# Optimization experiments

Hardware: AMD Instinct MI355X
Metric: run time of the kernel (lower is better)

Reference implementation:

```python
import jax, jax.numpy as jnp
import numpy as np

ALPHA = 0.1  # leaky relu negative slope
EF = 256     # edge_features

def setup_inputs() -> dict:
    key = jax.random.key(0)
    k1, k2, k3, k4, k5 = jax.random.split(key, 5)
    N, Na, IN_F, OUT_F = 8192, 8192, 512, 256 * 2 // 1  # OUT_F set below
    OUT_F = 512
    feat_edge   = jax.random.normal(k1, (N, EF), dtype=jnp.float32)
    feat_edge_a = jax.random.normal(k2, (Na, EF), dtype=jnp.float32)
    feat_node_a = jax.random.normal(k3, (Na, IN_F), dtype=jnp.float32)
    # xavier_normal-ish init for params
    weight = jax.random.normal(k4, (IN_F, OUT_F), dtype=jnp.float32) * (1.414 * np.sqrt(2.0 / (IN_F + OUT_F)))
    att    = jax.random.normal(k5, (2 * EF, 1), dtype=jnp.float32) * (1.414 * np.sqrt(2.0 / (2 * EF + 1)))
    return {"feat_edge": feat_edge, "feat_edge_a": feat_edge_a,
            "feat_node_a": feat_node_a, "weight": weight, "att": att}

def reference(feat_edge, feat_edge_a, feat_node_a, weight, att):
    # Wh: [Na, out_features]
    Wh = feat_node_a @ weight
    # additive attention scores via rank-1 broadcast: e [N, Na]
    s1 = feat_edge @ att[:EF, :]      # [N, 1]
    s2 = feat_edge_a @ att[EF:, :]    # [Na, 1]
    e = jax.nn.leaky_relu(s1 + s2.T, negative_slope=ALPHA)
    attention = jax.nn.softmax(e, axis=1)  # sup=False path; dropout identity (eval)
    h_prime = attention @ Wh               # [N, out_features]
    return jax.nn.elu(h_prime)             # concat=True -> elu
```

## Files before the change

### kernel.cpp

```cpp
#include <hip/hip_runtime.h>
#include <cstdint>
#include <cstddef>

#define LRALPHA 0.1f
static constexpr int NR = 8192;
static constexpr int EF = 256;
static constexpr int IN_F = 512;
static constexpr int OUT_F = 512;
static constexpr int KP2 = 1024;
static constexpr int NCH = 128;
static constexpr int CHR = 64;

typedef __attribute__((ext_vector_type(8))) _Float16 f16x8;
typedef __attribute__((ext_vector_type(4))) float f32x4;

__global__ __launch_bounds__(256) void k_prep(const float* __restrict__ feat_edge,
                                              const float* __restrict__ feat_edge_a,
                                              const float* __restrict__ att,
                                              const float* __restrict__ W,
                                              float* __restrict__ s1,
                                              float* __restrict__ s2,
                                              short* __restrict__ B3t) {
  int b = blockIdx.x;
  if (b < 4096) {
    int vrow = b * 4 + (threadIdx.x >> 6);
    int lane = threadIdx.x & 63;
    const float* feat; const float* av; float* outp; int row;
    if (vrow < NR) { row = vrow; feat = feat_edge; av = att; outp = s1; }
    else { row = vrow - NR; feat = feat_edge_a; av = att + EF; outp = s2; }
    float4 f = reinterpret_cast<const float4*>(feat + (size_t)row * EF)[lane];
    float4 a = reinterpret_cast<const float4*>(av)[lane];
    float d = f.x * a.x + f.y * a.y + f.z * a.z + f.w * a.w;
#pragma unroll
    for (int off = 32; off > 0; off >>= 1) d += __shfl_xor(d, off);
    if (lane == 0) outp[row] = d;
  } else {
    int i = (b - 4096) * 256 + threadIdx.x;
    int n = i >> 9, k = i & 511;
    float x = W[(size_t)k * OUT_F + n];
    _Float16 h = (_Float16)x;
    unsigned short u = __builtin_bit_cast(unsigned short, h);
    unsigned int w = (unsigned int)u | ((unsigned int)u << 16);
    *reinterpret_cast<unsigned int*>(B3t + (size_t)n * KP2 + 2 * k) = w;
  }
}

struct SReg4 { float4 a0, a1, a2, a3; int4 b0, b1, b2, b3; };

__device__ __forceinline__ int swz(int row, int slot) {
  return (row & ~7) | ((row & 7) ^ (slot & 7));
}

__global__ __launch_bounds__(256, 2) void k_gemm(const float* __restrict__ A,
                                                 const short* __restrict__ B3t,
                                                 float* __restrict__ Wh) {
  __shared__ short lA[2][8192];
  __shared__ short lB[2][8192];
  const int tid = threadIdx.x;
  const int wid = tid >> 6, lane = tid & 63;
  const int wr = wid >> 1, wc = wid & 1;
  int bid = blockIdx.x;
  int xcd = bid & 7, loc = bid >> 3;
  int mb = (xcd << 4) | (loc >> 3), nb = loc & 7;
  const int m0 = mb * 64, n0 = nb * 64;
  const int fr = lane & 15, g = lane >> 4;

  const int srow = tid >> 2, q = tid & 3;
  const float* gA = A + (size_t)(m0 + srow) * IN_F + q * 16;
  const short* gB = B3t + (size_t)(n0 + srow) * KP2 + q * 32;
  int wA[4], wB[4];
#pragma unroll
  for (int j = 0; j < 4; ++j) {
    int s = 4 * q + j;
    wA[j] = s * 512 + swz(srow, s) * 8;
    wB[j] = s * 512 + swz(srow, s) * 8;
  }

  f32x4 acc[2][2] = {};

  auto loadR = [&](SReg4& s, int t) {
    const float* pa = gA + t * 64;
    s.a0 = *reinterpret_cast<const float4*>(pa);
    s.a1 = *reinterpret_cast<const float4*>(pa + 4);
    s.a2 = *reinterpret_cast<const float4*>(pa + 8);
    s.a3 = *reinterpret_cast<const float4*>(pa + 12);
    const short* pb = gB + t * 128;
    s.b0 = *reinterpret_cast<const int4*>(pb);
    s.b1 = *reinterpret_cast<const int4*>(pb + 8);
    s.b2 = *reinterpret_cast<const int4*>(pb + 16);
    s.b3 = *reinterpret_cast<const int4*>(pb + 24);
  };

  auto cvt4 = [](float4 p) -> int4 {
    float xs[4] = {p.x, p.y, p.z, p.w};
    int out[4];
#pragma unroll
    for (int e = 0; e < 4; ++e) {
      _Float16 h = (_Float16)xs[e];
      _Float16 l = (_Float16)(xs[e] - (float)h);
      unsigned short uh = __builtin_bit_cast(unsigned short, h);
      unsigned short ul = __builtin_bit_cast(unsigned short, l);
      out[e] = (int)uh | ((int)ul << 16);
    }
    int4 r; r.x = out[0]; r.y = out[1]; r.z = out[2]; r.w = out[3];
    return r;
  };

  auto writeL = [&](int buf, SReg4& s) {
    *reinterpret_cast<int4*>(&lA[buf][wA[0]]) = cvt4(s.a0);
    *reinterpret_cast<int4*>(&lA[buf][wA[1]]) = cvt4(s.a1);
    *reinterpret_cast<int4*>(&lA[buf][wA[2]]) = cvt4(s.a2);
    *reinterpret_cast<int4*>(&lA[buf][wA[3]]) = cvt4(s.a3);
    *reinterpret_cast<int4*>(&lB[buf][wB[0]]) = s.b0;
    *reinterpret_cast<int4*>(&lB[buf][wB[1]]) = s.b1;
    *reinterpret_cast<int4*>(&lB[buf][wB[2]]) = s.b2;
    *reinterpret_cast<int4*>(&lB[buf][wB[3]]) = s.b3;
  };

  auto compute = [&](int buf) {
#pragma unroll
    for (int ks = 0; ks < 4; ++ks) {
      int s = ks * 4 + g;
      f16x8 af[2], bv[2];
#pragma unroll
      for (int m = 0; m < 2; ++m) {
        int row = wr * 32 + m * 16 + fr;
        af[m] = *reinterpret_cast<const f16x8*>(&lA[buf][s * 512 + swz(row, s) * 8]);
      }
#pragma unroll
      for (int n = 0; n < 2; ++n) {
        int row = wc * 32 + n * 16 + fr;
        bv[n] = *reinterpret_cast<const f16x8*>(&lB[buf][s * 512 + swz(row, s) * 8]);
      }
#pragma unroll
      for (int m = 0; m < 2; ++m)
#pragma unroll
        for (int n = 0; n < 2; ++n)
          acc[m][n] = __builtin_amdgcn_mfma_f32_16x16x32_f16(af[m], bv[n], acc[m][n], 0, 0, 0);
    }
  };

  SReg4 SA, SB;
  loadR(SA, 0); loadR(SB, 1);
  writeL(0, SA);
  loadR(SA, 2);
  __syncthreads();

  for (int t = 0; t < 4; t += 2) {
    writeL(1, SB); loadR(SB, t + 3);
    compute(0); __syncthreads();
    writeL(0, SA); loadR(SA, t + 4);
    compute(1); __syncthreads();
  }
  writeL(1, SB); loadR(SB, 7);
  compute(0); __syncthreads();
  writeL(0, SA);
  compute(1); __syncthreads();
  writeL(1, SB);
  compute(0); __syncthreads();
  compute(1);

#pragma unroll
  for (int m = 0; m < 2; ++m) {
#pragma unroll
    for (int n = 0; n < 2; ++n) {
      int row = m0 + wr * 32 + m * 16 + g * 4;
      int col = n0 + wc * 32 + n * 16 + fr;
#pragma unroll
      for (int r = 0; r < 4; ++r)
        Wh[(size_t)(row + r) * OUT_F + col] = acc[m][n][r];
    }
  }
}

__global__ __launch_bounds__(256) void k_rank(const float* __restrict__ s2,
                                              float* __restrict__ s2s, int* __restrict__ perm,
                                              float* __restrict__ eaA, float* __restrict__ ebA) {
  __shared__ unsigned int ls[32 * 260];
  int t = threadIdx.x;
#pragma unroll
  for (int k = 0; k < 8; ++k) {
    int q = t + 256 * k;
    int p = q >> 6, i = q & 63;
    uint4 u = reinterpret_cast<const uint4*>(s2)[q];
    uint4 v;
    v.x = (u.x >> 31) ? ~u.x : (u.x | 0x80000000u);
    v.y = (u.y >> 31) ? ~u.y : (u.y | 0x80000000u);
    v.z = (u.z >> 31) ? ~u.z : (u.z | 0x80000000u);
    v.w = (u.w >> 31) ? ~u.w : (u.w | 0x80000000u);
    *reinterpret_cast<uint4*>(&ls[p * 260 + i * 4]) = v;
  }
  __syncthreads();

  int ki = blockIdx.x * 8 + (t >> 5);
  int part = t & 31;
  unsigned int key = ls[(ki >> 8) * 260 + (ki & 255)];
  int rank = 0;
  const int base = part * 260;
  int jbase = part * 256;
#pragma unroll 8
  for (int q = 0; q < 64; ++q) {
    uint4 v = *reinterpret_cast<const uint4*>(&ls[base + q * 4]);
    int j = jbase + q * 4;
    rank += (v.x < key) || (v.x == key && (j + 0) < ki);
    rank += (v.y < key) || (v.y == key && (j + 1) < ki);
    rank += (v.z < key) || (v.z == key && (j + 2) < ki);
    rank += (v.w < key) || (v.w == key && (j + 3) < ki);
  }
  rank += __shfl_xor(rank, 1);
  rank += __shfl_xor(rank, 2);
  rank += __shfl_xor(rank, 4);
  rank += __shfl_xor(rank, 8);
  rank += __shfl_xor(rank, 16);
  if (part == 0) {
    float kf = s2[ki];
    s2s[rank] = kf; perm[rank] = ki;
    eaA[rank] = expf(kf); ebA[rank] = expf(LRALPHA * kf);
  }
}

__global__ __launch_bounds__(1024) void k_scan(const float* __restrict__ eaA,
                                               const float* __restrict__ ebA,
                                               float* __restrict__ sufa,
                                               float* __restrict__ preb) {
  int t = threadIdx.x;
  int lane = t & 63, w = t >> 6;
  float4 a0 = reinterpret_cast<const float4*>(eaA)[t * 2];
  float4 a1 = reinterpret_cast<const float4*>(eaA)[t * 2 + 1];
  float4 b0 = reinterpret_cast<const float4*>(ebA)[t * 2];
  float4 b1 = reinterpret_cast<const float4*>(ebA)[t * 2 + 1];
  float ea[8] = {a0.x, a0.y, a0.z, a0.w, a1.x, a1.y, a1.z, a1.w};
  float eb[8] = {b0.x, b0.y, b0.z, b0.w, b1.x, b1.y, b1.z, b1.w};
  float sa = 0.f, sb = 0.f;
#pragma unroll
  for (int e = 0; e < 8; ++e) { sa += ea[e]; sb += eb[e]; }

  float pb = sb;
#pragma unroll
  for (int off = 1; off < 64; off <<= 1) { float v = __shfl_up(pb, off); if (lane >= off) pb += v; }
  float pa = sa;
#pragma unroll
  for (int off = 1; off < 64; off <<= 1) { float v = __shfl_down(pa, off); if (lane < 64 - off) pa += v; }

  __shared__ float wtb[16], wta[16];
  if (lane == 63) wtb[w] = pb;
  if (lane == 0)  wta[w] = pa;
  __syncthreads();
  if (t == 0) {
    float rb = 0.f;
    for (int i = 0; i < 16; ++i) { float tmp = wtb[i]; wtb[i] = rb; rb += tmp; }
    float ra = 0.f;
    for (int i = 15; i >= 0; --i) { float tmp = wta[i]; wta[i] = ra; ra += tmp; }
  }
  __syncthreads();

  float run = wtb[w] + (pb - sb);
#pragma unroll
  for (int e = 0; e < 8; ++e) { preb[t * 8 + e] = run; run += eb[e]; }
  if (t == 1023) preb[NR] = run;
  run = wta[w] + (pa - sa);
#pragma unroll
  for (int e = 7; e >= 0; --e) { run += ea[e]; sufa[t * 8 + e] = run; }
  if (t == 0) sufa[NR] = 0.f;
}

__global__ __launch_bounds__(256) void k_passA(const float* __restrict__ Wh,
                                               const float* __restrict__ eaA,
                                               const float* __restrict__ ebA,
                                               const int* __restrict__ perm,
                                               float* __restrict__ chunkA, float* __restrict__ chunkB) {
  int chunk = blockIdx.x;
  int col = blockIdx.y * 256 + threadIdx.x;
  float accA = 0.f, accB = 0.f;
  int r0 = chunk * CHR;
  for (int rl = 0; rl < CHR; ++rl) {
    int r = r0 + rl;
    float v = Wh[(size_t)perm[r] * OUT_F + col];
    accA += eaA[r] * v;
    accB += ebA[r] * v;
  }
  chunkA[(size_t)col * NCH + chunk] = accA;
  chunkB[(size_t)col * NCH + chunk] = accB;
}

__global__ __launch_bounds__(256) void k_passB(const float* __restrict__ chunkA,
                                               const float* __restrict__ chunkB,
                                               float* __restrict__ baseA, float* __restrict__ baseB) {
  int lane = threadIdx.x & 63, w = threadIdx.x >> 6;
  int col = blockIdx.x * 4 + w;
  float xa0 = chunkA[(size_t)col * NCH + lane];
  float xa1 = chunkA[(size_t)col * NCH + 64 + lane];
  float yb0 = chunkB[(size_t)col * NCH + lane];
  float yb1 = chunkB[(size_t)col * NCH + 64 + lane];

  float p0 = yb0, p1 = yb1;
#pragma unroll
  for (int off = 1; off < 64; off <<= 1) {
    float v0 = __shfl_up(p0, off); if (lane >= off) p0 += v0;
    float v1 = __shfl_up(p1, off); if (lane >= off) p1 += v1;
  }
  float T0 = __shfl(p0, 63);
  p1 += T0;
  baseB[(size_t)lane * OUT_F + col] = p0 - yb0;
  baseB[(size_t)(64 + lane) * OUT_F + col] = p1 - yb1;

  float s0 = xa0, s1 = xa1;
#pragma unroll
  for (int off = 1; off < 64; off <<= 1) {
    float v1 = __shfl_down(s1, off); if (lane < 64 - off) s1 += v1;
    float v0 = __shfl_down(s0, off); if (lane < 64 - off) s0 += v0;
  }
  float S1 = __shfl(s1, 0);
  s0 += S1;
  baseA[(size_t)lane * OUT_F + col] = s0 - xa0;
  baseA[(size_t)(64 + lane) * OUT_F + col] = s1 - xa1;
}

__global__ __launch_bounds__(256) void k_passC(const float* __restrict__ Wh,
                                               const float* __restrict__ eaA,
                                               const float* __restrict__ ebA,
                                               const int* __restrict__ perm,
                                               const float* __restrict__ baseA,
                                               const float* __restrict__ baseB,
                                               float* __restrict__ SufA, float* __restrict__ PreB) {
  int chunk = blockIdx.x;
  int col = blockIdx.y * 256 + threadIdx.x;
  int r0 = chunk * CHR;
  float bA = baseA[(size_t)chunk * OUT_F + col];
  float bB = baseB[(size_t)chunk * OUT_F + col];
  float acc = 0.f;
  for (int rl = CHR - 1; rl >= 0; --rl) {
    int r = r0 + rl;
    float v = Wh[(size_t)perm[r] * OUT_F + col];
    acc += eaA[r] * v;
    SufA[(size_t)r * OUT_F + col] = acc + bA;
  }
  acc = 0.f;
  for (int rl = 0; rl < CHR; ++rl) {
    int r = r0 + rl;
    float v = Wh[(size_t)perm[r] * OUT_F + col];
    PreB[(size_t)r * OUT_F + col] = acc + bB;
    acc += ebA[r] * v;
  }
  if (chunk == NCH - 1) {
    SufA[(size_t)NR * OUT_F + col] = 0.f;
    PreB[(size_t)NR * OUT_F + col] = acc + bB;
  }
}

__global__ __launch_bounds__(256) void k_final(const float* __restrict__ s1,
                                               const float* __restrict__ s2s,
                                               const float* __restrict__ sufa,
                                               const float* __restrict__ preb,
                                               const float* __restrict__ SufA,
                                               const float* __restrict__ PreB,
                                               float* __restrict__ out) {
  int row = blockIdx.x * 4 + (threadIdx.x >> 6);
  int lane = threadIdx.x & 63;
  float sv = s1[row];
  float t = -sv;
  int lo = 0, hi = NR;
  while (lo < hi) {
    int mid = (lo + hi) >> 1;
    if (s2s[mid] > t) hi = mid; else lo = mid + 1;
  }
  float E1 = expf(sv), E1a = expf(LRALPHA * sv);
  float Z = E1 * sufa[lo] + E1a * preb[lo];
  const float* rA = SufA + (size_t)lo * OUT_F;
  const float* rB = PreB + (size_t)lo * OUT_F;
#pragma unroll
  for (int e = 0; e < 8; ++e) {
    int kc = e * 64 + lane;
    float num = E1 * rA[kc] + E1a * rB[kc];
    float h = num / Z;
    out[(size_t)row * OUT_F + kc] = (h > 0.f) ? h : expm1f(h);
  }
}

extern "C" void kernel_launch(void* const* d_in, const int* in_sizes, int n_in,
                              void* d_out, int out_size, void* d_ws, size_t ws_size,
                              hipStream_t stream) {
  (void)in_sizes; (void)n_in; (void)out_size; (void)ws_size;
  const float* feat_edge   = (const float*)d_in[0];
  const float* feat_edge_a = (const float*)d_in[1];
  const float* feat_node_a = (const float*)d_in[2];
  const float* weight      = (const float*)d_in[3];
  const float* att         = (const float*)d_in[4];
  float* out = (float*)d_out;

  char* ws = (char*)d_ws;
  size_t off = 0;
  auto alloc = [&](size_t bytes) { size_t o = off; off += (bytes + 255) & ~(size_t)255; return o; };

  float* Wh = (float*)(ws + alloc((size_t)NR * OUT_F * 4));
  size_t regionOff = alloc((size_t)(NR + 1) * OUT_F * 4 * 2);
  float* SufA = (float*)(ws + regionOff);
  float* PreB = (float*)(ws + regionOff + (size_t)(NR + 1) * OUT_F * 4);
  short* B3t  = (short*)(ws + regionOff);

  float* s1   = (float*)(ws + alloc(NR * 4));
  float* s2   = (float*)(ws + alloc(NR * 4));
  float* s2s  = (float*)(ws + alloc(NR * 4));
  int*   perm = (int*)  (ws + alloc(NR * 4));
  float* sufa = (float*)(ws + alloc((NR + 1) * 4));
  float* preb = (float*)(ws + alloc((NR + 1) * 4));
  float* eaA  = (float*)(ws + alloc(NR * 4));
  float* ebA  = (float*)(ws + alloc(NR * 4));
  float* chA  = (float*)(ws + alloc(NCH * OUT_F * 4));
  float* chB  = (float*)(ws + alloc(NCH * OUT_F * 4));
  float* bsA  = (float*)(ws + alloc(NCH * OUT_F * 4));
  float* bsB  = (float*)(ws + alloc(NCH * OUT_F * 4));

  k_prep<<<4096 + 1024, 256, 0, stream>>>(feat_edge, feat_edge_a, att, weight, s1, s2, B3t);
  k_gemm<<<1024, 256, 0, stream>>>(feat_node_a, B3t, Wh);
  k_rank<<<NR / 8, 256, 0, stream>>>(s2, s2s, perm, eaA, ebA);
  k_scan<<<1, 1024, 0, stream>>>(eaA, ebA, sufa, preb);
  k_passA<<<dim3(NCH, 2), 256, 0, stream>>>(Wh, eaA, ebA, perm, chA, chB);
  k_passB<<<NCH, 256, 0, stream>>>(chA, chB, bsA, bsB);
  k_passC<<<dim3(NCH, 2), 256, 0, stream>>>(Wh, eaA, ebA, perm, bsA, bsB, SufA, PreB);
  k_final<<<NR / 4, 256, 0, stream>>>(s1, s2s, sufa, preb, SufA, PreB, out);
}
```

Before: 86.30 us.

## Merge GEMM with rank kernel, fold scan and chunk-base pass into neighbours

Runs the GEMM and the s2 ranking sort as one launch, with blocks split by index over a shared LDS buffer. The global scalar scan moves into an extra block of passA, and passB is dropped because each passC block now sums the chunk totals it needs directly. Chunk totals are stored chunk-major for coalesced reads. This cuts three kernel launches and their serialisation gaps, but passC now does up to 128 redundant reads per column and the merged kernel carries the larger GEMM LDS footprint for rank blocks.

```diff
diff --git a/kernel.cpp b/kernel.cpp
--- a/kernel.cpp
+++ b/kernel.cpp
@@ -51,226 +51,231 @@
   return (row & ~7) | ((row & 7) ^ (slot & 7));
 }
 
-__global__ __launch_bounds__(256, 2) void k_gemm(const float* __restrict__ A,
-                                                 const short* __restrict__ B3t,
-                                                 float* __restrict__ Wh) {
-  __shared__ short lA[2][8192];
-  __shared__ short lB[2][8192];
+__global__ __launch_bounds__(256, 2) void k_gemmrank(const float* __restrict__ A,
+                                                     const short* __restrict__ B3t,
+                                                     float* __restrict__ Wh,
+                                                     const float* __restrict__ s2,
+                                                     float* __restrict__ s2s, int* __restrict__ perm,
+                                                     float* __restrict__ eaA, float* __restrict__ ebA) {
+  __shared__ int4 smem[4096];
   const int tid = threadIdx.x;
-  const int wid = tid >> 6, lane = tid & 63;
-  const int wr = wid >> 1, wc = wid & 1;
   int bid = blockIdx.x;
-  int xcd = bid & 7, loc = bid >> 3;
-  int mb = (xcd << 4) | (loc >> 3), nb = loc & 7;
-  const int m0 = mb * 64, n0 = nb * 64;
-  const int fr = lane & 15, g = lane >> 4;
-
-  const int srow = tid >> 2, q = tid & 3;
-  const float* gA = A + (size_t)(m0 + srow) * IN_F + q * 16;
-  const short* gB = B3t + (size_t)(n0 + srow) * KP2 + q * 32;
-  int wA[4], wB[4];
-#pragma unroll
-  for (int j = 0; j < 4; ++j) {
-    int s = 4 * q + j;
-    wA[j] = s * 512 + swz(srow, s) * 8;
-    wB[j] = s * 512 + swz(srow, s) * 8;
-  }
-
-  f32x4 acc[2][2] = {};
-
-  auto loadR = [&](SReg4& s, int t) {
-    const float* pa = gA + t * 64;
-    s.a0 = *reinterpret_cast<const float4*>(pa);
-    s.a1 = *reinterpret_cast<const float4*>(pa + 4);
-    s.a2 = *reinterpret_cast<const float4*>(pa + 8);
-    s.a3 = *reinterpret_cast<const float4*>(pa + 12);
-    const short* pb = gB + t * 128;
-    s.b0 = *reinterpret_cast<const int4*>(pb);
-    s.b1 = *reinterpret_cast<const int4*>(pb + 8);
-    s.b2 = *reinterpret_cast<const int4*>(pb + 16);
-    s.b3 = *reinterpret_cast<const int4*>(pb + 24);
-  };
-
-  auto cvt4 = [](float4 p) -> int4 {
-    float xs[4] = {p.x, p.y, p.z, p.w};
-    int out[4];
-#pragma unroll
-    for (int e = 0; e < 4; ++e) {
-      _Float16 h = (_Float16)xs[e];
-      _Float16 l = (_Float16)(xs[e] - (float)h);
-      unsigned short uh = __builtin_bit_cast(unsigned short, h);
-      unsigned short ul = __builtin_bit_cast(unsigned short, l);
-      out[e] = (int)uh | ((int)ul << 16);
-    }
-    int4 r; r.x = out[0]; r.y = out[1]; r.z = out[2]; r.w = out[3];
-    return r;
-  };
-
-  auto writeL = [&](int buf, SReg4& s) {
-    *reinterpret_cast<int4*>(&lA[buf][wA[0]]) = cvt4(s.a0);
-    *reinterpret_cast<int4*>(&lA[buf][wA[1]]) = cvt4(s.a1);
-    *reinterpret_cast<int4*>(&lA[buf][wA[2]]) = cvt4(s.a2);
-    *reinterpret_cast<int4*>(&lA[buf][wA[3]]) = cvt4(s.a3);
-    *reinterpret_cast<int4*>(&lB[buf][wB[0]]) = s.b0;
-    *reinterpret_cast<int4*>(&lB[buf][wB[1]]) = s.b1;
-    *reinterpret_cast<int4*>(&lB[buf][wB[2]]) = s.b2;
-    *reinterpret_cast<int4*>(&lB[buf][wB[3]]) = s.b3;
-  };
-
-  auto compute = [&](int buf) {
-#pragma unroll
-    for (int ks = 0; ks < 4; ++ks) {
-      int s = ks * 4 + g;
-      f16x8 af[2], bv[2];
-#pragma unroll
-      for (int m = 0; m < 2; ++m) {
-        int row = wr * 32 + m * 16 + fr;
-        af[m] = *reinterpret_cast<const f16x8*>(&lA[buf][s * 512 + swz(row, s) * 8]);
+  if (bid < 1024) {
+    short* lA = (short*)smem;
+    short* lB = (short*)smem + 16384;
+    const int wid = tid >> 6, lane = tid & 63;
+    const int wr = wid >> 1, wc = wid & 1;
+    int xcd = bid & 7, loc = bid >> 3;
+    int mb = (xcd << 4) | (loc >> 3), nb = loc & 7;
+    const int m0 = mb * 64, n0 = nb * 64;
+    const int fr = lane & 15, g = lane >> 4;
+
+    const int srow = tid >> 2, q = tid & 3;
+    const float* gA = A + (size_t)(m0 + srow) * IN_F + q * 16;
+    const short* gB = B3t + (size_t)(n0 + srow) * KP2 + q * 32;
+    int wA[4];
+#pragma unroll
+    for (int j = 0; j < 4; ++j) {
+      int s = 4 * q + j;
+      wA[j] = s * 512 + swz(srow, s) * 8;
+    }
+
+    f32x4 acc[2][2] = {};
+
+    auto loadR = [&](SReg4& s, int t) {
+      const float* pa = gA + t * 64;
+      s.a0 = *reinterpret_cast<const float4*>(pa);
+      s.a1 = *reinterpret_cast<const float4*>(pa + 4);
+      s.a2 = *reinterpret_cast<const float4*>(pa + 8);
+      s.a3 = *reinterpret_cast<const float4*>(pa + 12);
+      const short* pb = gB + t * 128;
+      s.b0 = *reinterpret_cast<const int4*>(pb);
+      s.b1 = *reinterpret_cast<const int4*>(pb + 8);
+      s.b2 = *reinterpret_cast<const int4*>(pb + 16);
+      s.b3 = *reinterpret_cast<const int4*>(pb + 24);
+    };
+
+    auto cvt4 = [](float4 p) -> int4 {
+      float xs[4] = {p.x, p.y, p.z, p.w};
+      int out[4];
+#pragma unroll
+      for (int e = 0; e < 4; ++e) {
+        _Float16 h = (_Float16)xs[e];
+        _Float16 l = (_Float16)(xs[e] - (float)h);
+        unsigned short uh = __builtin_bit_cast(unsigned short, h);
+        unsigned short ul = __builtin_bit_cast(unsigned short, l);
+        out[e] = (int)uh | ((int)ul << 16);
       }
+      int4 r; r.x = out[0]; r.y = out[1]; r.z = out[2]; r.w = out[3];
+      return r;
+    };
+
+    auto writeL = [&](int buf, SReg4& s) {
+      *reinterpret_cast<int4*>(&lA[buf * 8192 + wA[0]]) = cvt4(s.a0);
+      *reinterpret_cast<int4*>(&lA[buf * 8192 + wA[1]]) = cvt4(s.a1);
+      *reinterpret_cast<int4*>(&lA[buf * 8192 + wA[2]]) = cvt4(s.a2);
+      *reinterpret_cast<int4*>(&lA[buf * 8192 + wA[3]]) = cvt4(s.a3);
+      *reinterpret_cast<int4*>(&lB[buf * 8192 + wA[0]]) = s.b0;
+      *reinterpret_cast<int4*>(&lB[buf * 8192 + wA[1]]) = s.b1;
+      *reinterpret_cast<int4*>(&lB[buf * 8192 + wA[2]]) = s.b2;
+      *reinterpret_cast<int4*>(&lB[buf * 8192 + wA[3]]) = s.b3;
+    };
+
+    auto compute = [&](int buf) {
+#pragma unroll
+      for (int ks = 0; ks < 4; ++ks) {
+        int s = ks * 4 + g;
+        f16x8 af[2], bv[2];
+#pragma unroll
+        for (int m = 0; m < 2; ++m) {
+          int row = wr * 32 + m * 16 + fr;
+          af[m] = *reinterpret_cast<const f16x8*>(&lA[buf * 8192 + s * 512 + swz(row, s) * 8]);
+        }
+#pragma unroll
+        for (int n = 0; n < 2; ++n) {
+          int row = wc * 32 + n * 16 + fr;
+          bv[n] = *reinterpret_cast<const f16x8*>(&lB[buf * 8192 + s * 512 + swz(row, s) * 8]);
+        }
+#pragma unroll
+        for (int m = 0; m < 2; ++m)
+#pragma unroll
+          for (int n = 0; n < 2; ++n)
+            acc[m][n] = __builtin_amdgcn_mfma_f32_16x16x32_f16(af[m], bv[n], acc[m][n], 0, 0, 0);
+      }
+    };
+
+    SReg4 SA, SB;
+    loadR(SA, 0); loadR(SB, 1);
+    writeL(0, SA);
+    loadR(SA, 2);
+    __syncthreads();
+
+    for (int t = 0; t < 4; t += 2) {
+      writeL(1, SB); loadR(SB, t + 3);
+      compute(0); __syncthreads();
+      writeL(0, SA); loadR(SA, t + 4);
+      compute(1); __syncthreads();
+    }
+    writeL(1, SB); loadR(SB, 7);
+    compute(0); __syncthreads();
+    writeL(0, SA);
+    compute(1); __syncthreads();
+    writeL(1, SB);
+    compute(0); __syncthreads();
+    compute(1);
+
+#pragma unroll
+    for (int m = 0; m < 2; ++m) {
 #pragma unroll
       for (int n = 0; n < 2; ++n) {
-        int row = wc * 32 + n * 16 + fr;
-        bv[n] = *reinterpret_cast<const f16x8*>(&lB[buf][s * 512 + swz(row, s) * 8]);
+        int row = m0 + wr * 32 + m * 16 + g * 4;
+        int col = n0 + wc * 32 + n * 16 + fr;
+#pragma unroll
+        for (int r = 0; r < 4; ++r)
+          Wh[(size_t)(row + r) * OUT_F + col] = acc[m][n][r];
       }
-#pragma unroll
-      for (int m = 0; m < 2; ++m)
-#pragma unroll
-        for (int n = 0; n < 2; ++n)
-          acc[m][n] = __builtin_amdgcn_mfma_f32_16x16x32_f16(af[m], bv[n], acc[m][n], 0, 0, 0);
-    }
-  };
-
-  SReg4 SA, SB;
-  loadR(SA, 0); loadR(SB, 1);
-  writeL(0, SA);
-  loadR(SA, 2);
-  __syncthreads();
-
-  for (int t = 0; t < 4; t += 2) {
-    writeL(1, SB); loadR(SB, t + 3);
-    compute(0); __syncthreads();
-    writeL(0, SA); loadR(SA, t + 4);
-    compute(1); __syncthreads();
-  }
-  writeL(1, SB); loadR(SB, 7);
-  compute(0); __syncthreads();
-  writeL(0, SA);
-  compute(1); __syncthreads();
-  writeL(1, SB);
-  compute(0); __syncthreads();
-  compute(1);
-
-#pragma unroll
-  for (int m = 0; m < 2; ++m) {
-#pragma unroll
-    for (int n = 0; n < 2; ++n) {
-      int row = m0 + wr * 32 + m * 16 + g * 4;
-      int col = n0 + wc * 32 + n * 16 + fr;
-#pragma unroll
-      for (int r = 0; r < 4; ++r)
-        Wh[(size_t)(row + r) * OUT_F + col] = acc[m][n][r];
-    }
-  }
-}
-
-__global__ __launch_bounds__(256) void k_rank(const float* __restrict__ s2,
-                                              float* __restrict__ s2s, int* __restrict__ perm,
-                                              float* __restrict__ eaA, float* __restrict__ ebA) {
-  __shared__ unsigned int ls[32 * 260];
-  int t = threadIdx.x;
-#pragma unroll
-  for (int k = 0; k < 8; ++k) {
-    int q = t + 256 * k;
-    int p = q >> 6, i = q & 63;
-    uint4 u = reinterpret_cast<const uint4*>(s2)[q];
-    uint4 v;
-    v.x = (u.x >> 31) ? ~u.x : (u.x | 0x80000000u);
-    v.y = (u.y >> 31) ? ~u.y : (u.y | 0x80000000u);
-    v.z = (u.z >> 31) ? ~u.z : (u.z | 0x80000000u);
-    v.w = (u.w >> 31) ? ~u.w : (u.w | 0x80000000u);
-    *reinterpret_cast<uint4*>(&ls[p * 260 + i * 4]) = v;
-  }
-  __syncthreads();
-
-  int ki = blockIdx.x * 8 + (t >> 5);
-  int part = t & 31;
-  unsigned int key = ls[(ki >> 8) * 260 + (ki & 255)];
-  int rank = 0;
-  const int base = part * 260;
-  int jbase = part * 256;
+    }
+  } else {
+    unsigned int* ls = (unsigned int*)smem;
+#pragma unroll
+    for (int k = 0; k < 8; ++k) {
+      int q = tid + 256 * k;
+      int p = q >> 6, i = q & 63;
+      uint4 u = reinterpret_cast<const uint4*>(s2)[q];
+      uint4 v;
+      v.x = (u.x >> 31) ? ~u.x : (u.x | 0x80000000u);
+      v.y = (u.y >> 31) ? ~u.y : (u.y | 0x80000000u);
+      v.z = (u.z >> 31) ? ~u.z : (u.z | 0x80000000u);
+      v.w = (u.w >> 31) ? ~u.w : (u.w | 0x80000000u);
+      *reinterpret_cast<uint4*>(&ls[p * 260 + i * 4]) = v;
+    }
+    __syncthreads();
+
+    int ki = (bid - 1024) * 8 + (tid >> 5);
+    int part = tid & 31;
+    unsigned int key = ls[(ki >> 8) * 260 + (ki & 255)];
+    int rank = 0;
+    const int base = part * 260;
+    int jbase = part * 256;
 #pragma unroll 8
-  for (int q = 0; q < 64; ++q) {
-    uint4 v = *reinterpret_cast<const uint4*>(&ls[base + q * 4]);
-    int j = jbase + q * 4;
-    rank += (v.x < key) || (v.x == key && (j + 0) < ki);
-    rank += (v.y < key) || (v.y == key && (j + 1) < ki);
-    rank += (v.z < key) || (v.z == key && (j + 2) < ki);
-    rank += (v.w < key) || (v.w == key && (j + 3) < ki);
-  }
-  rank += __shfl_xor(rank, 1);
-  rank += __shfl_xor(rank, 2);
-  rank += __shfl_xor(rank, 4);
-  rank += __shfl_xor(rank, 8);
-  rank += __shfl_xor(rank, 16);
-  if (part == 0) {
-    float kf = s2[ki];
-    s2s[rank] = kf; perm[rank] = ki;
-    eaA[rank] = expf(kf); ebA[rank] = expf(LRALPHA * kf);
-  }
-}
-
-__global__ __launch_bounds__(1024) void k_scan(const float* __restrict__ eaA,
-                                               const float* __restrict__ ebA,
-                                               float* __restrict__ sufa,
-                                               float* __restrict__ preb) {
-  int t = threadIdx.x;
-  int lane = t & 63, w = t >> 6;
-  float4 a0 = reinterpret_cast<const float4*>(eaA)[t * 2];
-  float4 a1 = reinterpret_cast<const float4*>(eaA)[t * 2 + 1];
-  float4 b0 = reinterpret_cast<const float4*>(ebA)[t * 2];
-  float4 b1 = reinterpret_cast<const float4*>(ebA)[t * 2 + 1];
-  float ea[8] = {a0.x, a0.y, a0.z, a0.w, a1.x, a1.y, a1.z, a1.w};
-  float eb[8] = {b0.x, b0.y, b0.z, b0.w, b1.x, b1.y, b1.z, b1.w};
-  float sa = 0.f, sb = 0.f;
-#pragma unroll
-  for (int e = 0; e < 8; ++e) { sa += ea[e]; sb += eb[e]; }
-
-  float pb = sb;
-#pragma unroll
-  for (int off = 1; off < 64; off <<= 1) { float v = __shfl_up(pb, off); if (lane >= off) pb += v; }
-  float pa = sa;
-#pragma unroll
-  for (int off = 1; off < 64; off <<= 1) { float v = __shfl_down(pa, off); if (lane < 64 - off) pa += v; }
-
-  __shared__ float wtb[16], wta[16];
-  if (lane == 63) wtb[w] = pb;
-  if (lane == 0)  wta[w] = pa;
-  __syncthreads();
-  if (t == 0) {
-    float rb = 0.f;
-    for (int i = 0; i < 16; ++i) { float tmp = wtb[i]; wtb[i] = rb; rb += tmp; }
-    float ra = 0.f;
-    for (int i = 15; i >= 0; --i) { float tmp = wta[i]; wta[i] = ra; ra += tmp; }
-  }
-  __syncthreads();
-
-  float run = wtb[w] + (pb - sb);
-#pragma unroll
-  for (int e = 0; e < 8; ++e) { preb[t * 8 + e] = run; run += eb[e]; }
-  if (t == 1023) preb[NR] = run;
-  run = wta[w] + (pa - sa);
-#pragma unroll
-  for (int e = 7; e >= 0; --e) { run += ea[e]; sufa[t * 8 + e] = run; }
-  if (t == 0) sufa[NR] = 0.f;
+    for (int q = 0; q < 64; ++q) {
+      uint4 v = *reinterpret_cast<const uint4*>(&ls[base + q * 4]);
+      int j = jbase + q * 4;
+      rank += (v.x < key) || (v.x == key && (j + 0) < ki);
+      rank += (v.y < key) || (v.y == key && (j + 1) < ki);
+      rank += (v.z < key) || (v.z == key && (j + 2) < ki);
+      rank += (v.w < key) || (v.w == key && (j + 3) < ki);
+    }
+    rank += __shfl_xor(rank, 1);
+    rank += __shfl_xor(rank, 2);
+    rank += __shfl_xor(rank, 4);
+    rank += __shfl_xor(rank, 8);
+    rank += __shfl_xor(rank, 16);
+    if (part == 0) {
+      float kf = s2[ki];
+      s2s[rank] = kf; perm[rank] = ki;
+      eaA[rank] = expf(kf); ebA[rank] = expf(LRALPHA * kf);
+    }
+  }
 }
 
 __global__ __launch_bounds__(256) void k_passA(const float* __restrict__ Wh,
                                                const float* __restrict__ eaA,
                                                const float* __restrict__ ebA,
                                                const int* __restrict__ perm,
-                                               float* __restrict__ chunkA, float* __restrict__ chunkB) {
+                                               float* __restrict__ chunkA, float* __restrict__ chunkB,
+                                               float* __restrict__ sufa, float* __restrict__ preb) {
+  int t = threadIdx.x;
+  if (blockIdx.x == NCH) {
+    if (blockIdx.y != 0) return;
+    int lane = t & 63, w = t >> 6;
+    float sa = 0.f, sb = 0.f;
+#pragma unroll
+    for (int q = 0; q < 8; ++q) {
+      float4 va = reinterpret_cast<const float4*>(eaA)[t * 8 + q];
+      float4 vb = reinterpret_cast<const float4*>(ebA)[t * 8 + q];
+      sa += va.x + va.y + va.z + va.w;
+      sb += vb.x + vb.y + vb.z + vb.w;
+    }
+    float pb = sb;
+#pragma unroll
+    for (int off = 1; off < 64; off <<= 1) { float v = __shfl_up(pb, off); if (lane >= off) pb += v; }
+    float pa = sa;
+#pragma unroll
+    for (int off = 1; off < 64; off <<= 1) { float v = __shfl_down(pa, off); if (lane < 64 - off) pa += v; }
+    __shared__ float wtb[4], wta[4];
+    if (lane == 63) wtb[w] = pb;
+    if (lane == 0)  wta[w] = pa;
+    __syncthreads();
+    if (t == 0) {
+      float rb = 0.f;
+      for (int i = 0; i < 4; ++i) { float tmp = wtb[i]; wtb[i] = rb; rb += tmp; }
+      float ra = 0.f;
+      for (int i = 3; i >= 0; --i) { float tmp = wta[i]; wta[i] = ra; ra += tmp; }
+    }
+    __syncthreads();
+    float run = wtb[w] + (pb - sb);
+#pragma unroll
+    for (int q = 0; q < 8; ++q) {
+      float4 vb = reinterpret_cast<const float4*>(ebA)[t * 8 + q];
+      float e4[4] = {vb.x, vb.y, vb.z, vb.w};
+#pragma unroll
+      for (int e = 0; e < 4; ++e) { preb[t * 32 + q * 4 + e] = run; run += e4[e]; }
+    }
+    if (t == 255) preb[NR] = run;
+    run = wta[w] + (pa - sa);
+#pragma unroll
+    for (int q = 7; q >= 0; --q) {
+      float4 va = reinterpret_cast<const float4*>(eaA)[t * 8 + q];
+      float e4[4] = {va.x, va.y, va.z, va.w};
+#pragma unroll
+      for (int e = 3; e >= 0; --e) { run += e4[e]; sufa[t * 32 + q * 4 + e] = run; }
+    }
+    if (t == 0) sufa[NR] = 0.f;
+    return;
+  }
   int chunk = blockIdx.x;
-  int col = blockIdx.y * 256 + threadIdx.x;
+  int col = blockIdx.y * 256 + t;
   float accA = 0.f, accB = 0.f;
   int r0 = chunk * CHR;
   for (int rl = 0; rl < CHR; ++rl) {
@@ -279,55 +284,23 @@
     accA += eaA[r] * v;
     accB += ebA[r] * v;
   }
-  chunkA[(size_t)col * NCH + chunk] = accA;
-  chunkB[(size_t)col * NCH + chunk] = accB;
-}
-
-__global__ __launch_bounds__(256) void k_passB(const float* __restrict__ chunkA,
-                                               const float* __restrict__ chunkB,
-                                               float* __restrict__ baseA, float* __restrict__ baseB) {
-  int lane = threadIdx.x & 63, w = threadIdx.x >> 6;
-  int col = blockIdx.x * 4 + w;
-  float xa0 = chunkA[(size_t)col * NCH + lane];
-  float xa1 = chunkA[(size_t)col * NCH + 64 + lane];
-  float yb0 = chunkB[(size_t)col * NCH + lane];
-  float yb1 = chunkB[(size_t)col * NCH + 64 + lane];
-
-  float p0 = yb0, p1 = yb1;
-#pragma unroll
-  for (int off = 1; off < 64; off <<= 1) {
-    float v0 = __shfl_up(p0, off); if (lane >= off) p0 += v0;
-    float v1 = __shfl_up(p1, off); if (lane >= off) p1 += v1;
-  }
-  float T0 = __shfl(p0, 63);
-  p1 += T0;
-  baseB[(size_t)lane * OUT_F + col] = p0 - yb0;
-  baseB[(size_t)(64 + lane) * OUT_F + col] = p1 - yb1;
-
-  float s0 = xa0, s1 = xa1;
-#pragma unroll
-  for (int off = 1; off < 64; off <<= 1) {
-    float v1 = __shfl_down(s1, off); if (lane < 64 - off) s1 += v1;
-    float v0 = __shfl_down(s0, off); if (lane < 64 - off) s0 += v0;
-  }
-  float S1 = __shfl(s1, 0);
-  s0 += S1;
-  baseA[(size_t)lane * OUT_F + col] = s0 - xa0;
-  baseA[(size_t)(64 + lane) * OUT_F + col] = s1 - xa1;
+  chunkA[chunk * OUT_F + col] = accA;
+  chunkB[chunk * OUT_F + col] = accB;
 }
 
 __global__ __launch_bounds__(256) void k_passC(const float* __restrict__ Wh,
                                                const float* __restrict__ eaA,
                                                const float* __restrict__ ebA,
                                                const int* __restrict__ perm,
-                                               const float* __restrict__ baseA,
-                                               const float* __restrict__ baseB,
+                                               const float* __restrict__ chunkA,
+                                               const float* __restrict__ chunkB,
                                                float* __restrict__ SufA, float* __restrict__ PreB) {
   int chunk = blockIdx.x;
   int col = blockIdx.y * 256 + threadIdx.x;
+  float bA = 0.f, bB = 0.f;
+  for (int cp = chunk + 1; cp < NCH; ++cp) bA += chunkA[cp * OUT_F + col];
+  for (int cp = 0; cp < chunk; ++cp) bB += chunkB[cp * OUT_F + col];
   int r0 = chunk * CHR;
-  float bA = baseA[(size_t)chunk * OUT_F + col];
-  float bB = baseB[(size_t)chunk * OUT_F + col];
   float acc = 0.f;
   for (int rl = CHR - 1; rl >= 0; --rl) {
     int r = r0 + rl;
@@ -408,15 +381,10 @@
   float* ebA  = (float*)(ws + alloc(NR * 4));
   float* chA  = (float*)(ws + alloc(NCH * OUT_F * 4));
   float* chB  = (float*)(ws + alloc(NCH * OUT_F * 4));
-  float* bsA  = (float*)(ws + alloc(NCH * OUT_F * 4));
-  float* bsB  = (float*)(ws + alloc(NCH * OUT_F * 4));
 
   k_prep<<<4096 + 1024, 256, 0, stream>>>(feat_edge, feat_edge_a, att, weight, s1, s2, B3t);
-  k_gemm<<<1024, 256, 0, stream>>>(feat_node_a, B3t, Wh);
-  k_rank<<<NR / 8, 256, 0, stream>>>(s2, s2s, perm, eaA, ebA);
-  k_scan<<<1, 1024, 0, stream>>>(eaA, ebA, sufa, preb);
-  k_passA<<<dim3(NCH, 2), 256, 0, stream>>>(Wh, eaA, ebA, perm, chA, chB);
-  k_passB<<<NCH, 256, 0, stream>>>(chA, chB, bsA, bsB);
-  k_passC<<<dim3(NCH, 2), 256, 0, stream>>>(Wh, eaA, ebA, perm, bsA, bsB, SufA, PreB);
+  k_gemmrank<<<2048, 256, 0, stream>>>(feat_node_a, B3t, Wh, s2, s2s, perm, eaA, ebA);
+  k_passA<<<dim3(NCH + 1, 2), 256, 0, stream>>>(Wh, eaA, ebA, perm, chA, chB, sufa, preb);
+  k_passC<<<dim3(NCH, 2), 256, 0, stream>>>(Wh, eaA, ebA, perm, chA, chB, SufA, PreB);
   k_final<<<NR / 4, 256, 0, stream>>>(s1, s2s, sufa, preb, SufA, PreB, out);
 }
```

Result: slower. 107.7 us (+24.8%).
